# Optimization experiments

Measured on AMD Instinct MI355X. Metric: run time of the kernel, lower is better.

## Reference

```python
import jax, jax.numpy as jnp
import numpy as np

TEMPERATURE = 1.0  # registered buffer in the torch module
SOFTPLUS_SHIFT = 0.5413


def setup_inputs() -> dict:
    key = jax.random.key(0)
    k0, k1, k2, k3 = jax.random.split(key, 4)
    B, S, Din, Dout, T, DEP, H = 4, 2048, 1024, 512, 12, 3, 3
    L = 2 ** DEP
    return {
        "x": jax.random.normal(k0, (B, S, Din), jnp.float32),
        # normal(0, 0.1) init as in _init_forest_params
        "decision_weights": 0.1 * jax.random.normal(k1, (T, DEP, Din), jnp.float32),
        "decision_biases": jnp.zeros((T, DEP), jnp.float32),
        "node_temperature_logits": jnp.zeros((T, DEP), jnp.float32),
        "gate_w": jax.random.normal(k2, (T, Din), jnp.float32) / np.sqrt(Din),
        "gate_b": jnp.zeros((T,), jnp.float32),
        # xavier_normal over trailing (L, Dout) matrices
        "leaf_outputs": jax.random.normal(k3, (H, T, L, Dout), jnp.float32) * np.sqrt(2.0 / (L + Dout)),
    }


def _leaf_probs_depth3(decisions):
    # decisions: (B, S, T, 3) sigmoid routing probs; Kronecker product over 3 levels -> 8 leaves
    d0, d1, d2 = decisions[..., 0], decisions[..., 1], decisions[..., 2]
    p0 = jnp.stack([d0, 1.0 - d0], axis=-1)  # (B,S,T,2)
    p1 = jnp.stack([d1, 1.0 - d1], axis=-1)
    p2 = jnp.stack([d2, 1.0 - d2], axis=-1)
    B, S, T, _ = p0.shape
    lp = p0[..., :, None, None] * p1[..., None, :, None] * p2[..., None, None, :]
    return lp.reshape(B, S, T, 8)


def reference(x, decision_weights, decision_biases, node_temperature_logits, gate_w, gate_b, leaf_outputs):
    # decision logits per tree/level: (B,S,T,DEP)
    dec = jnp.einsum('bsd,tnd->bstn', x, decision_weights) + decision_biases
    node_temps = TEMPERATURE * jax.nn.softplus(node_temperature_logits + SOFTPLUS_SHIFT)  # (T,DEP)
    dec = jax.nn.sigmoid(dec / node_temps)
    leaf_probs = _leaf_probs_depth3(dec)  # (B,S,T,L)
    weights = jax.nn.softmax(x @ gate_w.T + gate_b, axis=-1)  # (B,S,T)
    # fused form of: per_tree = einsum('bstl,htld->hbstd'); out = einsum('hbstd,bst->hbsd')
    out = jnp.einsum('bstl,bst,htld->hbsd', leaf_probs, weights, leaf_outputs)
    # original returns list of per-head outputs; return stacked (H,B,S,Dout)
    return out
```

## Files before the change

kernel.cpp:

```cpp
#include <hip/hip_runtime.h>
#include <math.h>

#define NROWS 8192
#define DIN   1024
#define NT    12
#define NDEP  3
#define NDEC  36
#define NCOL  48
#define NC    96
#define NH    3
#define DOUT  512
#define CLP   104
#define LRP   52

typedef short bf16x8 __attribute__((ext_vector_type(8)));
typedef float f32x4  __attribute__((ext_vector_type(4)));

__device__ inline unsigned short f2bf(float f) {
    unsigned u = __float_as_uint(f);
    u = u + 0x7fff + ((u >> 16) & 1);
    return (unsigned short)(u >> 16);
}
__device__ inline float bf2f(unsigned short h) {
    return __uint_as_float(((unsigned)h) << 16);
}
__device__ inline unsigned cvt_pk(float a, float b) {
    unsigned r;
    asm("v_cvt_pk_bf16_f32 %0, %1, %2" : "=v"(r) : "v"(a), "v"(b));
    return r;
}
__device__ inline void split8(const float4 a, const float4 b, bf16x8& hi, bf16x8& lo) {
    union U { unsigned u[4]; bf16x8 v; };
    U H, L;
    H.u[0] = cvt_pk(a.x, a.y); H.u[1] = cvt_pk(a.z, a.w);
    H.u[2] = cvt_pk(b.x, b.y); H.u[3] = cvt_pk(b.z, b.w);
    const float r0 = a.x - __uint_as_float(H.u[0] << 16);
    const float r1 = a.y - __uint_as_float(H.u[0] & 0xffff0000u);
    const float r2 = a.z - __uint_as_float(H.u[1] << 16);
    const float r3 = a.w - __uint_as_float(H.u[1] & 0xffff0000u);
    const float r4 = b.x - __uint_as_float(H.u[2] << 16);
    const float r5 = b.y - __uint_as_float(H.u[2] & 0xffff0000u);
    const float r6 = b.z - __uint_as_float(H.u[3] << 16);
    const float r7 = b.w - __uint_as_float(H.u[3] & 0xffff0000u);
    L.u[0] = cvt_pk(r0, r1); L.u[1] = cvt_pk(r2, r3);
    L.u[2] = cvt_pk(r4, r5); L.u[3] = cvt_pk(r6, r7);
    hi = H.v; lo = L.v;
}

__global__ __launch_bounds__(256) void k_prep(const float* __restrict__ dw,
                                              const float* __restrict__ gw,
                                              const float* __restrict__ db,
                                              const float* __restrict__ ntl,
                                              const float* __restrict__ leaf,
                                              unsigned short* __restrict__ w_hi,
                                              unsigned short* __restrict__ w_lo,
                                              unsigned short* __restrict__ leafT,
                                              float* __restrict__ it_zb) {
    const int b = blockIdx.x;
    if (b < 192) {
        const int i = b * 256 + threadIdx.x;
        const int n = i >> 10;
        const float v = (n < NDEC) ? dw[i] : gw[i - NDEC * DIN];
        const unsigned short h = f2bf(v);
        w_hi[i] = h;
        w_lo[i] = f2bf(v - bf2f(h));
    } else if (b < 264) {
        const int i  = (b - 192) * 256 + threadIdx.x;
        const int hq = i % (NH * DOUT);
        const int kq = i / (NH * DOUT);
        const int h  = hq >> 9, d = hq & 511;
        bf16x8 v;
#pragma unroll
        for (int e = 0; e < 8; ++e)
            v[e] = (short)f2bf(leaf[(size_t)(h * NC + kq * 8 + e) * DOUT + d]);
        *(bf16x8*)(leafT + (size_t)hq * NC + kq * 8) = v;
    } else {
        const int i = threadIdx.x;
        if (i < NDEC) {
            const float v  = ntl[i] + 0.5413f;
            const float sp = (v > 20.0f) ? v : logf(1.0f + expf(v));
            const float it = 1.0f / sp;
            it_zb[i]        = it;
            it_zb[NDEC + i] = db[i] * it;
        }
    }
}

__global__ __launch_bounds__(512) void k_fused(const float* __restrict__ x,
                                               const unsigned short* __restrict__ w_hi,
                                               const unsigned short* __restrict__ w_lo,
                                               const unsigned short* __restrict__ leafT,
                                               const float* __restrict__ it_zb,
                                               const float* __restrict__ gb,
                                               float* __restrict__ out) {
    __shared__ __align__(16) float Lred[8][16][LRP];
    __shared__ __align__(16) unsigned short Cl[16][CLP];

    const int tid  = threadIdx.x;
    const int wv   = tid >> 6, lane = tid & 63;
    const int m    = lane & 15;
    const int kq   = lane >> 4;
    const int row0 = blockIdx.x * 16;

    f32x4 acc[3];
#pragma unroll
    for (int nf = 0; nf < 3; ++nf)
#pragma unroll
        for (int r = 0; r < 4; ++r) acc[nf][r] = 0.0f;

    const float*          xp  = x    + (size_t)(row0 + m) * DIN + wv * 128 + kq * 8;
    const unsigned short* whp = w_hi + (size_t)m * DIN + wv * 128 + kq * 8;
    const unsigned short* wlp = w_lo + (size_t)m * DIN + wv * 128 + kq * 8;

#pragma unroll
    for (int ks = 0; ks < 4; ++ks) {
        const float4 xa = *(const float4*)(xp + ks * 32);
        const float4 xb = *(const float4*)(xp + ks * 32 + 4);
        bf16x8 xhi, xlo;
        split8(xa, xb, xhi, xlo);
#pragma unroll
        for (int nf = 0; nf < 3; ++nf) {
            const bf16x8 whi = *(const bf16x8*)(whp + (size_t)nf * 16 * DIN + ks * 32);
            const bf16x8 wlo = *(const bf16x8*)(wlp + (size_t)nf * 16 * DIN + ks * 32);
            acc[nf] = __builtin_amdgcn_mfma_f32_16x16x32_bf16(whi, xhi, acc[nf], 0, 0, 0);
            acc[nf] = __builtin_amdgcn_mfma_f32_16x16x32_bf16(whi, xlo, acc[nf], 0, 0, 0);
            acc[nf] = __builtin_amdgcn_mfma_f32_16x16x32_bf16(wlo, xhi, acc[nf], 0, 0, 0);
        }
    }
#pragma unroll
    for (int nf = 0; nf < 3; ++nf)
        *(f32x4*)&Lred[wv][m][nf * 16 + kq * 4] = acc[nf];
    __syncthreads();

    if (tid < 256) {
        const int erow = tid >> 4;
        const int slot = tid & 15;
        float lg0 = 0.f, lg1 = 0.f, lg2 = 0.f, g = -1e30f;
        if (slot < NT) {
            float lgg = 0.f;
#pragma unroll
            for (int w = 0; w < 8; ++w) {
                lg0 += Lred[w][erow][slot * 3 + 0];
                lg1 += Lred[w][erow][slot * 3 + 1];
                lg2 += Lred[w][erow][slot * 3 + 2];
                lgg += Lred[w][erow][NDEC + slot];
            }
            g = lgg + gb[slot];
        }
        float mx = g;
#pragma unroll
        for (int off = 1; off < 16; off <<= 1) mx = fmaxf(mx, __shfl_xor(mx, off, 16));
        const float e = (slot < NT) ? expf(g - mx) : 0.f;
        float s = e;
#pragma unroll
        for (int off = 1; off < 16; off <<= 1) s += __shfl_xor(s, off, 16);
        if (slot < NT) {
            const float wt = e * __builtin_amdgcn_rcpf(s);
            const float z0 = lg0 * it_zb[slot * 3 + 0] + it_zb[NDEC + slot * 3 + 0];
            const float z1 = lg1 * it_zb[slot * 3 + 1] + it_zb[NDEC + slot * 3 + 1];
            const float z2 = lg2 * it_zb[slot * 3 + 2] + it_zb[NDEC + slot * 3 + 2];
            const float d0 = __builtin_amdgcn_rcpf(1.0f + expf(-z0));
            const float d1 = __builtin_amdgcn_rcpf(1.0f + expf(-z1));
            const float d2 = __builtin_amdgcn_rcpf(1.0f + expf(-z2));
            float c[8];
#pragma unroll
            for (int l = 0; l < 8; ++l) {
                const float p0 = (l & 4) ? (1.0f - d0) : d0;
                const float p1 = (l & 2) ? (1.0f - d1) : d1;
                const float p2 = (l & 1) ? (1.0f - d2) : d2;
                c[l] = wt * p0 * p1 * p2;
            }
            union { unsigned u[4]; bf16x8 v; } P;
            P.u[0] = cvt_pk(c[0], c[1]); P.u[1] = cvt_pk(c[2], c[3]);
            P.u[2] = cvt_pk(c[4], c[5]); P.u[3] = cvt_pk(c[6], c[7]);
            *(bf16x8*)&Cl[erow][slot * 8] = P.v;
        }
    }
    __syncthreads();

    bf16x8 cfr[3];
#pragma unroll
    for (int ks = 0; ks < 3; ++ks)
        cfr[ks] = *(const bf16x8*)&Cl[m][ks * 32 + kq * 8];

#pragma unroll
    for (int i = 0; i < 12; ++i) {
        const int f   = wv * 12 + i;
        const int h   = f >> 5;
        const int d0c = (f & 31) * 16;
        const unsigned short* bp = leafT + ((size_t)h * DOUT + d0c + m) * NC + kq * 8;
        f32x4 a;
#pragma unroll
        for (int r = 0; r < 4; ++r) a[r] = 0.0f;
#pragma unroll
        for (int ks = 0; ks < 3; ++ks) {
            const bf16x8 lfr = *(const bf16x8*)(bp + ks * 32);
            a = __builtin_amdgcn_mfma_f32_16x16x32_bf16(lfr, cfr[ks], a, 0, 0, 0);
        }
        *(f32x4*)(out + ((size_t)h * NROWS + row0 + m) * DOUT + d0c + kq * 4) = a;
    }
}

extern "C" void kernel_launch(void* const* d_in, const int* in_sizes, int n_in,
                              void* d_out, int out_size, void* d_ws, size_t ws_size,
                              hipStream_t stream) {
    const float* x    = (const float*)d_in[0];
    const float* dw   = (const float*)d_in[1];
    const float* db   = (const float*)d_in[2];
    const float* ntl  = (const float*)d_in[3];
    const float* gw   = (const float*)d_in[4];
    const float* gb   = (const float*)d_in[5];
    const float* leaf = (const float*)d_in[6];
    float* out = (float*)d_out;

    char* ws = (char*)d_ws;
    unsigned short* w_hi  = (unsigned short*)(ws);
    unsigned short* w_lo  = (unsigned short*)(ws + 98304);
    unsigned short* leafT = (unsigned short*)(ws + 196608);
    float*          it_zb = (float*)(ws + 491520);

    k_prep<<<265, 256, 0, stream>>>(dw, gw, db, ntl, leaf, w_hi, w_lo, leafT, it_zb);
    k_fused<<<NROWS / 16, 512, 0, stream>>>(x, w_hi, w_lo, leafT, it_zb, gb, out);
}
```

Baseline: 42.76 us.

## Split fused kernel into routing-coefficient kernel and leaf-output GEMM kernel

Splits the single fused kernel in two. The first computes the gated leaf-probability coefficients and writes them in bf16 to a global workspace. The second reads them and runs the leaf-output MFMA on a 2D grid, giving six times more blocks for the write-heavy output stage. This aims to raise parallelism and store bandwidth for the 48 MB fp32 output, at the cost of an extra launch and a global round trip for the coefficients; the first-stage K loop is also only partially unrolled.

New measurement: 46.95 us. +9.8%, slower.

```diff
diff --git a/kernel.cpp b/kernel.cpp
--- a/kernel.cpp
+++ b/kernel.cpp
@@ -10,7 +10,6 @@
 #define NC    96
 #define NH    3
 #define DOUT  512
-#define CLP   104
 #define LRP   52
 
 typedef short bf16x8 __attribute__((ext_vector_type(8)));
@@ -86,15 +85,13 @@
     }
 }
 
-__global__ __launch_bounds__(512) void k_fused(const float* __restrict__ x,
-                                               const unsigned short* __restrict__ w_hi,
-                                               const unsigned short* __restrict__ w_lo,
-                                               const unsigned short* __restrict__ leafT,
-                                               const float* __restrict__ it_zb,
-                                               const float* __restrict__ gb,
-                                               float* __restrict__ out) {
+__global__ __launch_bounds__(512) void k_A(const float* __restrict__ x,
+                                           const unsigned short* __restrict__ w_hi,
+                                           const unsigned short* __restrict__ w_lo,
+                                           const float* __restrict__ it_zb,
+                                           const float* __restrict__ gb,
+                                           unsigned short* __restrict__ Cg) {
     __shared__ __align__(16) float Lred[8][16][LRP];
-    __shared__ __align__(16) unsigned short Cl[16][CLP];
 
     const int tid  = threadIdx.x;
     const int wv   = tid >> 6, lane = tid & 63;
@@ -112,7 +109,7 @@
     const unsigned short* whp = w_hi + (size_t)m * DIN + wv * 128 + kq * 8;
     const unsigned short* wlp = w_lo + (size_t)m * DIN + wv * 128 + kq * 8;
 
-#pragma unroll
+#pragma unroll 2
     for (int ks = 0; ks < 4; ++ks) {
         const float4 xa = *(const float4*)(xp + ks * 32);
         const float4 xb = *(const float4*)(xp + ks * 32 + 4);
@@ -173,22 +170,33 @@
             union { unsigned u[4]; bf16x8 v; } P;
             P.u[0] = cvt_pk(c[0], c[1]); P.u[1] = cvt_pk(c[2], c[3]);
             P.u[2] = cvt_pk(c[4], c[5]); P.u[3] = cvt_pk(c[6], c[7]);
-            *(bf16x8*)&Cl[erow][slot * 8] = P.v;
-        }
-    }
-    __syncthreads();
+            *(bf16x8*)(Cg + (size_t)(row0 + erow) * NC + slot * 8) = P.v;
+        }
+    }
+}
+
+__global__ __launch_bounds__(256) void k_B(const unsigned short* __restrict__ Cg,
+                                           const unsigned short* __restrict__ leafT,
+                                           float* __restrict__ out) {
+    const int tid   = threadIdx.x;
+    const int wv    = tid >> 6, lane = tid & 63;
+    const int m     = lane & 15;
+    const int kq    = lane >> 4;
+    const int row0  = blockIdx.x * 16;
+    const int fbase = blockIdx.y * 16 + wv * 4;
 
     bf16x8 cfr[3];
+    const unsigned short* cp = Cg + (size_t)(row0 + m) * NC + kq * 8;
 #pragma unroll
     for (int ks = 0; ks < 3; ++ks)
-        cfr[ks] = *(const bf16x8*)&Cl[m][ks * 32 + kq * 8];
-
-#pragma unroll
-    for (int i = 0; i < 12; ++i) {
-        const int f   = wv * 12 + i;
-        const int h   = f >> 5;
-        const int d0c = (f & 31) * 16;
-        const unsigned short* bp = leafT + ((size_t)h * DOUT + d0c + m) * NC + kq * 8;
+        cfr[ks] = *(const bf16x8*)(cp + ks * 32);
+
+#pragma unroll
+    for (int i = 0; i < 4; ++i) {
+        const int f  = fbase + i;
+        const int h  = f >> 5;
+        const int d0 = (f & 31) * 16;
+        const unsigned short* bp = leafT + ((size_t)h * DOUT + d0 + m) * NC + kq * 8;
         f32x4 a;
 #pragma unroll
         for (int r = 0; r < 4; ++r) a[r] = 0.0f;
@@ -197,7 +205,7 @@
             const bf16x8 lfr = *(const bf16x8*)(bp + ks * 32);
             a = __builtin_amdgcn_mfma_f32_16x16x32_bf16(lfr, cfr[ks], a, 0, 0, 0);
         }
-        *(f32x4*)(out + ((size_t)h * NROWS + row0 + m) * DOUT + d0c + kq * 4) = a;
+        *(f32x4*)(out + ((size_t)h * NROWS + row0 + m) * DOUT + d0 + kq * 4) = a;
     }
 }
 
@@ -218,7 +226,9 @@
     unsigned short* w_lo  = (unsigned short*)(ws + 98304);
     unsigned short* leafT = (unsigned short*)(ws + 196608);
     float*          it_zb = (float*)(ws + 491520);
+    unsigned short* Cg    = (unsigned short*)(ws + 524288);
 
     k_prep<<<265, 256, 0, stream>>>(dw, gw, db, ntl, leaf, w_hi, w_lo, leafT, it_zb);
-    k_fused<<<NROWS / 16, 512, 0, stream>>>(x, w_hi, w_lo, leafT, it_zb, gb, out);
-}
+    k_A<<<NROWS / 16, 512, 0, stream>>>(x, w_hi, w_lo, it_zb, gb, Cg);
+    k_B<<<dim3(NROWS / 16, 6), 256, 0, stream>>>(Cg, leafT, out);
+}
```
